# Kernel optimization log

Hardware: AMD Instinct MI355X
Metric: run time of the kernel (lower is better)

The kernel has to match this reference:

```python
import jax, jax.numpy as jnp
import numpy as np

NEG_INF = -1.0e9
LEAKY_SLOPE = 0.2


def setup_inputs() -> dict:
    key = jax.random.key(0)
    k1, k2, k3, k4, k5 = jax.random.split(key, 5)
    B, N, F_in, H, D = 4, 2048, 128, 4, 32
    x = jax.random.normal(k1, (B, N, F_in), dtype=jnp.float32)
    # binary adjacency; force self-loops so every row has >=1 neighbour
    adj = jax.random.randint(k2, (N, N), 0, 2).astype(jnp.float32)
    adj = jnp.maximum(adj, jnp.eye(N, dtype=jnp.float32))
    W = jax.random.normal(k3, (H, F_in, D), dtype=jnp.float32) * (1.0 / np.sqrt(F_in))
    a_left = jax.random.normal(k4, (H, D, 1), dtype=jnp.float32) * (1.0 / np.sqrt(D))
    a_right = jax.random.normal(k5, (H, D, 1), dtype=jnp.float32) * (1.0 / np.sqrt(D))
    bias = jnp.zeros((H, D), dtype=jnp.float32)
    return {"x": x, "adj": adj, "W": W, "a_left": a_left, "a_right": a_right, "bias": bias}


def reference(x, adj, W, a_left, a_right, bias):
    # x: (B,N,F) ; W: (H,F,D) -> h: (B,H,N,D)
    h = jnp.einsum('bnf,hfd->bhnd', x, W)
    # separable additive scores: (B,H,N)
    al = jnp.einsum('bhnd,hd->bhn', h, a_left[..., 0])
    ar = jnp.einsum('bhnd,hd->bhn', h, a_right[..., 0])
    e = al[:, :, :, None] + ar[:, :, None, :]          # (B,H,N,N)
    e = jnp.where(e >= 0, e, LEAKY_SLOPE * e)           # LeakyReLU(0.2)
    mask = adj[None, None] > 0.5
    e = jnp.where(mask, e, NEG_INF)
    alpha = jax.nn.softmax(e, axis=-1)                  # (B,H,N,N)
    # inference: dropout on alpha is identity
    out = jnp.einsum('bhmn,bhnd->bhmd', alpha, h) + bias[None, :, None, :]
    out = jax.nn.elu(out)
    # concat heads: (B,H,N,D) -> (B,N,H*D)
    B, H, N, D = out.shape
    out = jnp.transpose(out, (0, 2, 1, 3)).reshape(B, N, H * D)
    return out
```

## Files before the change

kernel.cpp:

```cpp
#include <hip/hip_runtime.h>
#include <hip/hip_bf16.h>

#define Bn 4
#define Nn 2048
#define Fn 128
#define Hn 4
#define Dn 32
#define LOG2E 1.44269504f

typedef __attribute__((ext_vector_type(4))) float f32x4;
typedef __attribute__((ext_vector_type(8))) short s16x8;
typedef __attribute__((ext_vector_type(4))) short s16x4;
typedef _Float16 f16x8 __attribute__((ext_vector_type(8)));

__device__ __forceinline__ short f2h(float f) {
  _Float16 h = (_Float16)f;
  return __builtin_bit_cast(short, h);
}

__global__ __launch_bounds__(256) void k_pack(
    const float* __restrict__ adj, const float* __restrict__ W,
    unsigned long long* __restrict__ adjbits, short* __restrict__ Wt)
{
  const int blk = blockIdx.x;
  const int t = threadIdx.x;
  if (blk < Nn) {
    const int wv = t >> 6, lane = t & 63;
    const float* ap = adj + (size_t)blk * Nn;
    #pragma unroll
    for (int s = 0; s < 8; ++s) {
      const int n0 = (wv * 8 + s) * 64;
      const unsigned long long m = __ballot(ap[n0 + lane] > 0.5f);
      if (lane == 0) adjbits[blk * 32 + wv * 8 + s] = m;
    }
  } else {
    const int h = blk - Nn;
    const float* Wp = W + h * Fn * Dn;
    #pragma unroll
    for (int i = 0; i < 16; i += 4) {
      const int idx = t * 16 + i;
      const f32x4 w4 = *(const f32x4*)(Wp + idx);
      const int k = idx >> 5, d0 = idx & 31;
      #pragma unroll
      for (int j = 0; j < 4; ++j)
        Wt[(h * Dn + d0 + j) * Fn + k] = f2h(w4[j]);
    }
  }
}

__global__ __launch_bounds__(64) void k_proj(
    const float* __restrict__ x, const short* __restrict__ Wt,
    const float* __restrict__ aL, const float* __restrict__ aR,
    float* __restrict__ al, float* __restrict__ ar, short* __restrict__ ht)
{
  const int m0 = blockIdx.x * 16;
  const int b = m0 >> 11, nloc = m0 & 2047;
  const int lane = threadIdx.x;
  const int r = lane & 15, g = lane >> 4;

  const float* xp = x + (size_t)(m0 + r) * Fn + g * 8;
  f32x4 c[8] = {};
  #pragma unroll
  for (int ks = 0; ks < 4; ++ks) {
    const f32x4 xa = *(const f32x4*)(xp + ks * 32);
    const f32x4 xb = *(const f32x4*)(xp + ks * 32 + 4);
    f16x8 af;
    #pragma unroll
    for (int j = 0; j < 4; ++j) { af[j] = (_Float16)xa[j]; af[j + 4] = (_Float16)xb[j]; }
    const short* wp = Wt + r * Fn + ks * 32 + g * 8;
    #pragma unroll
    for (int cf = 0; cf < 8; ++cf) {
      const f16x8 bf = __builtin_bit_cast(f16x8, *(const s16x8*)(wp + cf * 16 * Fn));
      c[cf] = __builtin_amdgcn_mfma_f32_16x16x32_f16(af, bf, c[cf], 0, 0, 0);
    }
  }

  float vl[16] = {}, vr[16] = {};
  #pragma unroll
  for (int cf = 0; cf < 8; ++cf) {
    const int hh = cf >> 1;
    const float aLv = aL[hh * Dn + (cf & 1) * 16 + r] * LOG2E;
    const float aRv = aR[hh * Dn + (cf & 1) * 16 + r] * LOG2E;
    #pragma unroll
    for (int q = 0; q < 4; ++q) {
      vl[hh * 4 + q] = fmaf(c[cf][q], aLv, vl[hh * 4 + q]);
      vr[hh * 4 + q] = fmaf(c[cf][q], aRv, vr[hh * 4 + q]);
    }
  }
  #pragma unroll
  for (int i = 0; i < 16; ++i) {
    #pragma unroll
    for (int st = 1; st < 16; st <<= 1) {
      vl[i] += __shfl_xor(vl[i], st);
      vr[i] += __shfl_xor(vr[i], st);
    }
  }
  float ol = vl[0], orr = vr[0];
  #pragma unroll
  for (int i = 1; i < 16; ++i) {
    ol  = (r == i) ? vl[i] : ol;
    orr = (r == i) ? vr[i] : orr;
  }
  const int hh = r >> 2, qq = r & 3;
  al[(size_t)(b * Hn + hh) * Nn + nloc + g * 4 + qq] = ol;
  ar[(size_t)(b * Hn + hh) * Nn + nloc + g * 4 + qq] = orr;

  #pragma unroll
  for (int cf = 0; cf < 8; ++cf) {
    const int hd = cf >> 1, d = (cf & 1) * 16 + r;
    s16x4 hv;
    #pragma unroll
    for (int q = 0; q < 4; ++q) hv[q] = f2h(c[cf][q]);
    *(s16x4*)(ht + ((size_t)(b * Hn + hd) * Dn + d) * Nn + nloc + g * 4) = hv;
  }
}

__global__ __launch_bounds__(512, 4) void k_attn(
    const unsigned long long* __restrict__ adjbits,
    const float* __restrict__ al, const float* __restrict__ ar,
    const short* __restrict__ ht, const float* __restrict__ bias,
    float* __restrict__ out)
{
  __shared__ float ar_s[Nn];
  __shared__ float accS[8][16][32];
  __shared__ float lS[8][16];

  const int blk = blockIdx.x;
  const int mt = blk & 127, bh = blk >> 7;
  const int b = bh >> 2, head = bh & 3;
  const int m0 = mt * 16;
  const int t = threadIdx.x;
  const int wv = t >> 6, lane = t & 63;
  const int r = lane & 15, g = lane >> 4;

  ((f32x4*)ar_s)[t] = ((const f32x4*)(ar + (size_t)bh * Nn))[t];

  const unsigned long long abits = adjbits[(size_t)(m0 + r) * 32 + wv * 4 + g];
  const float al_m = al[(size_t)bh * Nn + m0 + r] - 4.0f;

  const short* htA = ht + ((size_t)bh * Dn + r) * Nn + wv * 256 + g * 64;
  const short* htB = htA + 16 * Nn;
  s16x8 hA0 = *(const s16x8*)(htA);      s16x8 hB0 = *(const s16x8*)(htB);
  s16x8 hA1 = *(const s16x8*)(htA + 8);  s16x8 hB1 = *(const s16x8*)(htB + 8);
  s16x8 hA2 = *(const s16x8*)(htA + 16); s16x8 hB2 = *(const s16x8*)(htB + 16);
  s16x8 hA3 = *(const s16x8*)(htA + 24); s16x8 hB3 = *(const s16x8*)(htB + 24);
  s16x8 hA4 = *(const s16x8*)(htA + 32); s16x8 hB4 = *(const s16x8*)(htB + 32);
  s16x8 hA5 = *(const s16x8*)(htA + 40); s16x8 hB5 = *(const s16x8*)(htB + 40);
  s16x8 hA6 = *(const s16x8*)(htA + 48); s16x8 hB6 = *(const s16x8*)(htB + 48);
  s16x8 hA7 = *(const s16x8*)(htA + 56); s16x8 hB7 = *(const s16x8*)(htB + 56);

  __syncthreads();

  const float* arp = ar_s + wv * 256 + g * 64;
  float ps = 0.f;
  f32x4 accA = {0.f,0.f,0.f,0.f}, accB = {0.f,0.f,0.f,0.f};

  #define CHUNK(ci, hAx, hBx)                                                  \
  {                                                                            \
    const f32x4 a0 = *(const f32x4*)(arp + ci * 8);                            \
    const f32x4 a1 = *(const f32x4*)(arp + ci * 8 + 4);                        \
    const unsigned int byte = (unsigned int)(abits >> (ci * 8)) & 0xffu;       \
    float p[8];                                                                \
    _Pragma("unroll")                                                          \
    for (int j = 0; j < 4; ++j) {                                              \
      const float s0 = al_m + a0[j];                                           \
      const float s1 = al_m + a1[j];                                           \
      const float e0 = exp2f(fmaxf(s0, fmaf(0.2f, s0, -3.2f)));                \
      const float e1 = exp2f(fmaxf(s1, fmaf(0.2f, s1, -3.2f)));                \
      p[j]     = (byte & (1u << j))       ? e0 : 0.f;                          \
      p[j + 4] = (byte & (1u << (j + 4))) ? e1 : 0.f;                          \
    }                                                                          \
    _Pragma("unroll")                                                          \
    for (int j = 0; j < 8; ++j) ps += p[j];                                    \
    f16x8 pf;                                                                  \
    _Pragma("unroll")                                                          \
    for (int j = 0; j < 8; ++j) pf[j] = (_Float16)p[j];                        \
    accA = __builtin_amdgcn_mfma_f32_16x16x32_f16(                             \
        pf, __builtin_bit_cast(f16x8, hAx), accA, 0, 0, 0);                    \
    accB = __builtin_amdgcn_mfma_f32_16x16x32_f16(                             \
        pf, __builtin_bit_cast(f16x8, hBx), accB, 0, 0, 0);                    \
  }

  CHUNK(0, hA0, hB0) CHUNK(1, hA1, hB1) CHUNK(2, hA2, hB2) CHUNK(3, hA3, hB3)
  CHUNK(4, hA4, hB4) CHUNK(5, hA5, hB5) CHUNK(6, hA6, hB6) CHUNK(7, hA7, hB7)
  #undef CHUNK

  ps += __shfl_xor(ps, 16);
  ps += __shfl_xor(ps, 32);

  #pragma unroll
  for (int q = 0; q < 4; ++q) {
    accS[wv][4 * g + q][r]      = accA[q];
    accS[wv][4 * g + q][r + 16] = accB[q];
  }
  if (g == 0) lS[wv][r] = ps;
  __syncthreads();

  const int row = t >> 5, dc = t & 31;
  float L = 0.f, v = 0.f;
  #pragma unroll
  for (int w = 0; w < 8; ++w) { L += lS[w][row]; v += accS[w][row][dc]; }
  v = v / L + bias[head * Dn + dc];
  v = v > 0.f ? v : __expf(v) - 1.f;
  out[((size_t)b * Nn + m0 + row) * (Hn * Dn) + head * Dn + dc] = v;
}

extern "C" void kernel_launch(void* const* d_in, const int* in_sizes, int n_in,
                              void* d_out, int out_size, void* d_ws, size_t ws_size,
                              hipStream_t stream) {
  const float* x    = (const float*)d_in[0];
  const float* adj  = (const float*)d_in[1];
  const float* W    = (const float*)d_in[2];
  const float* aL   = (const float*)d_in[3];
  const float* aR   = (const float*)d_in[4];
  const float* bias = (const float*)d_in[5];
  float* out = (float*)d_out;

  float* al = (float*)d_ws;
  float* ar = al + (Bn * Hn) * Nn;
  short* ht = (short*)(ar + (Bn * Hn) * Nn);
  unsigned long long* adjbits =
      (unsigned long long*)(ht + (size_t)(Bn * Hn) * Dn * Nn);
  short* Wt = (short*)(adjbits + Nn * (Nn / 64));

  hipLaunchKernelGGL(k_pack, dim3(Nn + Hn), dim3(256), 0, stream, adj, W, adjbits, Wt);
  hipLaunchKernelGGL(k_proj, dim3((Bn * Nn) / 16), dim3(64), 0, stream,
                     x, Wt, aL, aR, al, ar, ht);
  hipLaunchKernelGGL(k_attn, dim3((Bn * Hn) * (Nn / 16)), dim3(512), 0, stream,
                     adjbits, al, ar, ht, bias, out);
}
```

Before: 122.6 us.

## Fold attention vectors into weights and compute row sums via MFMA

Precomputes W·a_left and W·a_right per head in the pack kernel, so the projection kernel gets al/ar from one extra MFMA instead of a long shuffle reduction. In the attention kernel, the softmax denominator is accumulated with an MFMA against a ones vector instead of scalar adds plus shuffles. The change also pads the shared-memory arrays to avoid bank conflicts, uses the raw hardware exp2, and lowers the occupancy hint on k_attn. Rounding W·a to fp16 and summing fp16-rounded probabilities adds small precision changes to the logits and the normaliser.

```diff
diff --git a/kernel.cpp b/kernel.cpp
--- a/kernel.cpp
+++ b/kernel.cpp
@@ -20,7 +20,9 @@
 
 __global__ __launch_bounds__(256) void k_pack(
     const float* __restrict__ adj, const float* __restrict__ W,
-    unsigned long long* __restrict__ adjbits, short* __restrict__ Wt)
+    const float* __restrict__ aL, const float* __restrict__ aR,
+    unsigned long long* __restrict__ adjbits, short* __restrict__ Wt,
+    short* __restrict__ Waux)
 {
   const int blk = blockIdx.x;
   const int t = threadIdx.x;
@@ -33,24 +35,38 @@
       const unsigned long long m = __ballot(ap[n0 + lane] > 0.5f);
       if (lane == 0) adjbits[blk * 32 + wv * 8 + s] = m;
     }
-  } else {
+  } else if (t < 128) {
     const int h = blk - Nn;
-    const float* Wp = W + h * Fn * Dn;
-    #pragma unroll
-    for (int i = 0; i < 16; i += 4) {
-      const int idx = t * 16 + i;
-      const f32x4 w4 = *(const f32x4*)(Wp + idx);
-      const int k = idx >> 5, d0 = idx & 31;
+    const int f = t;
+    const float* Wp = W + ((size_t)h * Fn + f) * Dn;
+    float wv[32];
+    float dl = 0.f, dr = 0.f;
+    #pragma unroll
+    for (int d4 = 0; d4 < 8; ++d4) {
+      const f32x4 w4 = *(const f32x4*)(Wp + d4 * 4);
       #pragma unroll
-      for (int j = 0; j < 4; ++j)
-        Wt[(h * Dn + d0 + j) * Fn + k] = f2h(w4[j]);
-    }
-  }
-}
-
-__global__ __launch_bounds__(64) void k_proj(
+      for (int j = 0; j < 4; ++j) {
+        const int d = d4 * 4 + j;
+        wv[d] = w4[j];
+        dl = fmaf(w4[j], aL[h * Dn + d], dl);
+        dr = fmaf(w4[j], aR[h * Dn + d], dr);
+      }
+    }
+    #pragma unroll
+    for (int d = 0; d < 32; ++d)
+      Wt[(h * Dn + d) * Fn + f] = f2h(wv[d]);
+    Waux[(h * 2 + 0) * Fn + f] = f2h(dl * LOG2E);
+    Waux[(h * 2 + 1) * Fn + f] = f2h(dr * LOG2E);
+    if (h == 0) {
+      #pragma unroll
+      for (int cc = 8; cc < 16; ++cc) Waux[cc * Fn + f] = 0;
+    }
+  }
+}
+
+__global__ void k_proj(
     const float* __restrict__ x, const short* __restrict__ Wt,
-    const float* __restrict__ aL, const float* __restrict__ aR,
+    const short* __restrict__ Waux,
     float* __restrict__ al, float* __restrict__ ar, short* __restrict__ ht)
 {
   const int m0 = blockIdx.x * 16;
@@ -60,6 +76,7 @@
 
   const float* xp = x + (size_t)(m0 + r) * Fn + g * 8;
   f32x4 c[8] = {};
+  f32x4 caux = {};
   #pragma unroll
   for (int ks = 0; ks < 4; ++ks) {
     const f32x4 xa = *(const f32x4*)(xp + ks * 32);
@@ -73,37 +90,9 @@
       const f16x8 bf = __builtin_bit_cast(f16x8, *(const s16x8*)(wp + cf * 16 * Fn));
       c[cf] = __builtin_amdgcn_mfma_f32_16x16x32_f16(af, bf, c[cf], 0, 0, 0);
     }
-  }
-
-  float vl[16] = {}, vr[16] = {};
-  #pragma unroll
-  for (int cf = 0; cf < 8; ++cf) {
-    const int hh = cf >> 1;
-    const float aLv = aL[hh * Dn + (cf & 1) * 16 + r] * LOG2E;
-    const float aRv = aR[hh * Dn + (cf & 1) * 16 + r] * LOG2E;
-    #pragma unroll
-    for (int q = 0; q < 4; ++q) {
-      vl[hh * 4 + q] = fmaf(c[cf][q], aLv, vl[hh * 4 + q]);
-      vr[hh * 4 + q] = fmaf(c[cf][q], aRv, vr[hh * 4 + q]);
-    }
-  }
-  #pragma unroll
-  for (int i = 0; i < 16; ++i) {
-    #pragma unroll
-    for (int st = 1; st < 16; st <<= 1) {
-      vl[i] += __shfl_xor(vl[i], st);
-      vr[i] += __shfl_xor(vr[i], st);
-    }
-  }
-  float ol = vl[0], orr = vr[0];
-  #pragma unroll
-  for (int i = 1; i < 16; ++i) {
-    ol  = (r == i) ? vl[i] : ol;
-    orr = (r == i) ? vr[i] : orr;
-  }
-  const int hh = r >> 2, qq = r & 3;
-  al[(size_t)(b * Hn + hh) * Nn + nloc + g * 4 + qq] = ol;
-  ar[(size_t)(b * Hn + hh) * Nn + nloc + g * 4 + qq] = orr;
+    const f16x8 ba = __builtin_bit_cast(f16x8, *(const s16x8*)(Waux + r * Fn + ks * 32 + g * 8));
+    caux = __builtin_amdgcn_mfma_f32_16x16x32_f16(af, ba, caux, 0, 0, 0);
+  }
 
   #pragma unroll
   for (int cf = 0; cf < 8; ++cf) {
@@ -113,16 +102,24 @@
     for (int q = 0; q < 4; ++q) hv[q] = f2h(c[cf][q]);
     *(s16x4*)(ht + ((size_t)(b * Hn + hd) * Dn + d) * Nn + nloc + g * 4) = hv;
   }
-}
-
-__global__ __launch_bounds__(512, 4) void k_attn(
+
+  if (r < 8) {
+    const int hh = r >> 1;
+    float* dst = (r & 1) ? ar : al;
+    #pragma unroll
+    for (int q = 0; q < 4; ++q)
+      dst[(size_t)(b * Hn + hh) * Nn + nloc + g * 4 + q] = caux[q];
+  }
+}
+
+__global__ __launch_bounds__(512, 2) void k_attn(
     const unsigned long long* __restrict__ adjbits,
     const float* __restrict__ al, const float* __restrict__ ar,
     const short* __restrict__ ht, const float* __restrict__ bias,
     float* __restrict__ out)
 {
-  __shared__ float ar_s[Nn];
-  __shared__ float accS[8][16][32];
+  __shared__ float ar_s[32][68];
+  __shared__ float accS[8][16][33];
   __shared__ float lS[8][16];
 
   const int blk = blockIdx.x;
@@ -133,7 +130,10 @@
   const int wv = t >> 6, lane = t & 63;
   const int r = lane & 15, g = lane >> 4;
 
-  ((f32x4*)ar_s)[t] = ((const f32x4*)(ar + (size_t)bh * Nn))[t];
+  {
+    const f32x4 av = ((const f32x4*)(ar + (size_t)bh * Nn))[t];
+    *(f32x4*)&ar_s[t >> 4][(t & 15) * 4] = av;
+  }
 
   const unsigned long long abits = adjbits[(size_t)(m0 + r) * 32 + wv * 4 + g];
   const float al_m = al[(size_t)bh * Nn + m0 + r] - 4.0f;
@@ -148,12 +148,18 @@
   s16x8 hA5 = *(const s16x8*)(htA + 40); s16x8 hB5 = *(const s16x8*)(htB + 40);
   s16x8 hA6 = *(const s16x8*)(htA + 48); s16x8 hB6 = *(const s16x8*)(htB + 48);
   s16x8 hA7 = *(const s16x8*)(htA + 56); s16x8 hB7 = *(const s16x8*)(htB + 56);
+  asm volatile("" :: "v"(hA0), "v"(hA1), "v"(hA2), "v"(hA3),
+                     "v"(hA4), "v"(hA5), "v"(hA6), "v"(hA7),
+                     "v"(hB0), "v"(hB1), "v"(hB2), "v"(hB3),
+                     "v"(hB4), "v"(hB5), "v"(hB6), "v"(hB7));
 
   __syncthreads();
 
-  const float* arp = ar_s + wv * 256 + g * 64;
-  float ps = 0.f;
+  const float* arp = &ar_s[wv * 4 + g][0];
   f32x4 accA = {0.f,0.f,0.f,0.f}, accB = {0.f,0.f,0.f,0.f};
+  f32x4 accL = {0.f,0.f,0.f,0.f};
+  const f16x8 onesB = {(_Float16)1.f, (_Float16)1.f, (_Float16)1.f, (_Float16)1.f,
+                       (_Float16)1.f, (_Float16)1.f, (_Float16)1.f, (_Float16)1.f};
 
   #define CHUNK(ci, hAx, hBx)                                                  \
   {                                                                            \
@@ -165,13 +171,11 @@
     for (int j = 0; j < 4; ++j) {                                              \
       const float s0 = al_m + a0[j];                                           \
       const float s1 = al_m + a1[j];                                           \
-      const float e0 = exp2f(fmaxf(s0, fmaf(0.2f, s0, -3.2f)));                \
-      const float e1 = exp2f(fmaxf(s1, fmaf(0.2f, s1, -3.2f)));                \
+      const float e0 = __builtin_amdgcn_exp2f(fmaxf(s0, fmaf(0.2f, s0, -3.2f))); \
+      const float e1 = __builtin_amdgcn_exp2f(fmaxf(s1, fmaf(0.2f, s1, -3.2f))); \
       p[j]     = (byte & (1u << j))       ? e0 : 0.f;                          \
       p[j + 4] = (byte & (1u << (j + 4))) ? e1 : 0.f;                          \
     }                                                                          \
-    _Pragma("unroll")                                                          \
-    for (int j = 0; j < 8; ++j) ps += p[j];                                    \
     f16x8 pf;                                                                  \
     _Pragma("unroll")                                                          \
     for (int j = 0; j < 8; ++j) pf[j] = (_Float16)p[j];                        \
@@ -179,21 +183,22 @@
         pf, __builtin_bit_cast(f16x8, hAx), accA, 0, 0, 0);                    \
     accB = __builtin_amdgcn_mfma_f32_16x16x32_f16(                             \
         pf, __builtin_bit_cast(f16x8, hBx), accB, 0, 0, 0);                    \
+    accL = __builtin_amdgcn_mfma_f32_16x16x32_f16(pf, onesB, accL, 0, 0, 0);   \
   }
 
   CHUNK(0, hA0, hB0) CHUNK(1, hA1, hB1) CHUNK(2, hA2, hB2) CHUNK(3, hA3, hB3)
   CHUNK(4, hA4, hB4) CHUNK(5, hA5, hB5) CHUNK(6, hA6, hB6) CHUNK(7, hA7, hB7)
   #undef CHUNK
 
-  ps += __shfl_xor(ps, 16);
-  ps += __shfl_xor(ps, 32);
-
   #pragma unroll
   for (int q = 0; q < 4; ++q) {
     accS[wv][4 * g + q][r]      = accA[q];
     accS[wv][4 * g + q][r + 16] = accB[q];
   }
-  if (g == 0) lS[wv][r] = ps;
+  if (r == 0) {
+    #pragma unroll
+    for (int q = 0; q < 4; ++q) lS[wv][4 * g + q] = accL[q];
+  }
   __syncthreads();
 
   const int row = t >> 5, dc = t & 31;
@@ -222,10 +227,12 @@
   unsigned long long* adjbits =
       (unsigned long long*)(ht + (size_t)(Bn * Hn) * Dn * Nn);
   short* Wt = (short*)(adjbits + Nn * (Nn / 64));
-
-  hipLaunchKernelGGL(k_pack, dim3(Nn + Hn), dim3(256), 0, stream, adj, W, adjbits, Wt);
+  short* Waux = Wt + (Hn * Dn) * Fn;
+
+  hipLaunchKernelGGL(k_pack, dim3(Nn + Hn), dim3(256), 0, stream,
+                     adj, W, aL, aR, adjbits, Wt, Waux);
   hipLaunchKernelGGL(k_proj, dim3((Bn * Nn) / 16), dim3(64), 0, stream,
-                     x, Wt, aL, aR, al, ar, ht);
+                     x, Wt, Waux, al, ar, ht);
   hipLaunchKernelGGL(k_attn, dim3((Bn * Hn) * (Nn / 16)), dim3(512), 0, stream,
                      adjbits, al, ar, ht, bias, out);
 }
```

New measurement: 122.5 us. About the same (-0.1%).
